# Kernel tuning notes

Measured on AMD Instinct MI355X. Metric: run time of the kernel, lower is better.

The kernel has to match this reference:

```python
import jax, jax.numpy as jnp
import numpy as np

EMBED_DIM = 768
NUM_HEADS = 12
HEAD_DIM = EMBED_DIM // NUM_HEADS
SCALE = HEAD_DIM ** -0.5
EPS = 1e-5


def _layernorm(x, g, b):
    m = jnp.mean(x, axis=-1, keepdims=True)
    v = jnp.mean(jnp.square(x - m), axis=-1, keepdims=True)
    return (x - m) * jax.lax.rsqrt(v + EPS) * g + b


def setup_inputs() -> dict:
    key = jax.random.key(0)
    ks = jax.random.split(key, 8)
    B, N, D, Hd = 16, 1024, EMBED_DIM, HEAD_DIM
    x = jax.random.normal(ks[0], (B, N, D), dtype=jnp.float32)
    W_qkv = jax.random.normal(ks[1], (D, 3 * D), dtype=jnp.float32) * (D ** -0.5)
    b_qkv = jnp.zeros((3 * D,), dtype=jnp.float32)
    W_proj = jax.random.normal(ks[2], (D, D), dtype=jnp.float32) * (D ** -0.5)
    b_proj = jnp.zeros((D,), dtype=jnp.float32)
    return {
        "x": x,
        "ln_g": jnp.ones((D,), jnp.float32), "ln_b": jnp.zeros((D,), jnp.float32),
        "W_qkv": W_qkv, "b_qkv": b_qkv,
        "qn_g": jnp.ones((Hd,), jnp.float32), "qn_b": jnp.zeros((Hd,), jnp.float32),
        "kn_g": jnp.ones((Hd,), jnp.float32), "kn_b": jnp.zeros((Hd,), jnp.float32),
        "W_proj": W_proj, "b_proj": b_proj,
    }


def reference(x, ln_g, ln_b, W_qkv, b_qkv, qn_g, qn_b, kn_g, kn_b, W_proj, b_proj):
    B, N, D = x.shape
    H, Hd = NUM_HEADS, HEAD_DIM
    xn = _layernorm(x, ln_g, ln_b)                      # qkv_norm (pre-LN of embed_dim)
    qkv = xn @ W_qkv + b_qkv                            # [B,N,3D]
    qkv = qkv.reshape(B, N, 3, H, Hd)
    q = jnp.transpose(qkv[:, :, 0], (0, 2, 1, 3))       # [B,H,N,Hd]
    k = jnp.transpose(qkv[:, :, 1], (0, 2, 1, 3))
    v = jnp.transpose(qkv[:, :, 2], (0, 2, 1, 3))
    q = _layernorm(q, qn_g, qn_b)                       # per-head QK LayerNorm
    k = _layernorm(k, kn_g, kn_b)
    attn = jnp.einsum("bhnd,bhmd->bhnm", q, k) * SCALE
    attn = jax.nn.softmax(attn, axis=-1)
    out = jnp.einsum("bhnm,bhmd->bhnd", attn, v)        # [B,H,N,Hd]
    out = jnp.transpose(out, (0, 2, 1, 3)).reshape(B, N, D)
    return out @ W_proj + b_proj
```

## Files before the change

### kernel.cpp

```cpp
#include <hip/hip_runtime.h>

typedef _Float16 half8 __attribute__((ext_vector_type(8)));
typedef _Float16 half4 __attribute__((ext_vector_type(4)));
typedef _Float16 half2v __attribute__((ext_vector_type(2)));
typedef float f32x4 __attribute__((ext_vector_type(4)));

#define B_    16
#define N_    1024
#define D_    768
#define H_    12
#define M_    (B_ * N_)
#define QKVN_ 2304
#define EPS_  1e-5f
#define QS_   0.18033688011112042f

__device__ __forceinline__ float exp2_fast(float x) {
#if __has_builtin(__builtin_amdgcn_exp2f)
    return __builtin_amdgcn_exp2f(x);
#else
    return __builtin_exp2f(x);
#endif
}

__device__ __forceinline__ size_t pk(int t16, int kc, int lg, int p, int e) {
    return ((size_t)(t16 * 24 + kc) * 4 + lg) * 128 + p * 8 + e;
}

__global__ __launch_bounds__(256) void convert_w(const float* __restrict__ Wqkv,
                                                 const float* __restrict__ Wproj,
                                                 _Float16* __restrict__ wqkv_p,
                                                 _Float16* __restrict__ wproj_p) {
    int idx = blockIdx.x * 256 + threadIdx.x;
    const int n1 = D_ * QKVN_;
    int k, n; float v; _Float16* dst;
    if (idx < n1) { k = idx / QKVN_; n = idx % QKVN_; v = Wqkv[idx]; dst = wqkv_p; }
    else { int r = idx - n1; k = r / D_; n = r % D_; v = Wproj[r]; dst = wproj_p; }
    dst[pk(n >> 4, k >> 5, (k >> 3) & 3, n & 15, k & 7)] = (_Float16)v;
}

__global__ __launch_bounds__(256) void ln_embed(const float* __restrict__ x,
                                                const float* __restrict__ g,
                                                const float* __restrict__ bb,
                                                _Float16* __restrict__ xp) {
    int row = blockIdx.x;
    int tid = threadIdx.x;
    const float2* xr = (const float2*)(x + (size_t)row * D_);
    float2 v0 = xr[tid];
    float2 v1 = make_float2(0.f, 0.f);
    if (tid < 128) v1 = xr[256 + tid];
    float s = v0.x + v0.y + v1.x + v1.y;
    float q = v0.x * v0.x + v0.y * v0.y + v1.x * v1.x + v1.y * v1.y;
#pragma unroll
    for (int m = 32; m >= 1; m >>= 1) {
        s += __shfl_xor(s, m);
        q += __shfl_xor(q, m);
    }
    __shared__ float ss[4], qq[4];
    int wave = tid >> 6;
    if ((tid & 63) == 0) { ss[wave] = s; qq[wave] = q; }
    __syncthreads();
    float S = ss[0] + ss[1] + ss[2] + ss[3];
    float Q = qq[0] + qq[1] + qq[2] + qq[3];
    float mean = S * (1.f / 768.f);
    float var  = Q * (1.f / 768.f) - mean * mean;
    float rstd = rsqrtf(var + EPS_);
    const float2* g2 = (const float2*)g;
    const float2* b2 = (const float2*)bb;
    int mt = row >> 4, p = row & 15;
    {
        int d0 = 2 * tid;
        float2 ga = g2[tid], ba = b2[tid];
        half2v w;
        w[0] = (_Float16)((v0.x - mean) * rstd * ga.x + ba.x);
        w[1] = (_Float16)((v0.y - mean) * rstd * ga.y + ba.y);
        *(half2v*)&xp[pk(mt, d0 >> 5, (d0 >> 3) & 3, p, d0 & 7)] = w;
    }
    if (tid < 128) {
        int d0 = 512 + 2 * tid;
        float2 ga = g2[256 + tid], ba = b2[256 + tid];
        half2v w;
        w[0] = (_Float16)((v1.x - mean) * rstd * ga.x + ba.x);
        w[1] = (_Float16)((v1.y - mean) * rstd * ga.y + ba.y);
        *(half2v*)&xp[pk(mt, d0 >> 5, (d0 >> 3) & 3, p, d0 & 7)] = w;
    }
}

__global__ __launch_bounds__(256, 3) void gemm_qkv(const _Float16* __restrict__ Ap,
                                                   const _Float16* __restrict__ Bp,
                                                   const float* __restrict__ bias,
                                                   const float* __restrict__ qn_g,
                                                   const float* __restrict__ qn_b,
                                                   const float* __restrict__ kn_g,
                                                   const float* __restrict__ kn_b,
                                                   _Float16* __restrict__ qo,
                                                   _Float16* __restrict__ ko,
                                                   _Float16* __restrict__ vt) {
    int xcd = blockIdx.x & 7, loc = blockIdx.x >> 3;
    int mt0 = (xcd * 16 + loc / 18) * 8;
    int nt0 = (loc % 18) * 8;
    int tid = threadIdx.x;
    int wave = tid >> 6, lane = tid & 63;
    int wm = wave >> 1, wn = wave & 1;
    int lg = lane >> 4, l15 = lane & 15;

    const _Float16* pa[4];
    const _Float16* pb[4];
#pragma unroll
    for (int i = 0; i < 4; ++i) {
        pa[i] = Ap + (size_t)(mt0 + wm * 4 + i) * 12288 + lane * 8;
        pb[i] = Bp + (size_t)(nt0 + wn * 4 + i) * 12288 + lane * 8;
    }
    f32x4 acc[4][4] = {};
    half8 a0[4], b0[4], a1[4], b1[4];
    auto ld = [&](half8 (&a)[4], half8 (&b)[4], int t) {
        int off = t * 512;
#pragma unroll
        for (int i = 0; i < 4; ++i) {
            a[i] = *(const half8*)(pa[i] + off);
            b[i] = *(const half8*)(pb[i] + off);
        }
    };
    auto mm = [&](half8 (&a)[4], half8 (&b)[4]) {
#pragma unroll
        for (int mi = 0; mi < 4; ++mi)
#pragma unroll
            for (int ni = 0; ni < 4; ++ni)
                acc[mi][ni] = __builtin_amdgcn_mfma_f32_16x16x32_f16(a[mi], b[ni], acc[mi][ni], 0, 0, 0);
    };
    ld(a0, b0, 0);
    for (int tt = 0; tt < 11; ++tt) {
        ld(a1, b1, 2 * tt + 1);
        mm(a0, b0);
        ld(a0, b0, 2 * tt + 2);
        mm(a1, b1);
    }
    ld(a1, b1, 23);
    mm(a0, b0);
    mm(a1, b1);

    int m0 = mt0 * 16, n0 = nt0 * 16;
    int col0 = n0 + wn * 64;
    int s = col0 / 768;
    int hcol = (col0 % 768) >> 6;
    float qkvb[4];
#pragma unroll
    for (int ni = 0; ni < 4; ++ni) qkvb[ni] = bias[col0 + ni * 16 + l15];

    if (s == 2) {
#pragma unroll
        for (int mi = 0; mi < 4; ++mi) {
            int r0 = m0 + wm * 64 + mi * 16 + lg * 4;
            int bidx = r0 >> 10, pos = r0 & 1023;
            int kvblk = pos >> 5, h = (pos >> 4) & 1, lgR = (pos >> 2) & 3;
            size_t vbase = ((size_t)(bidx * H_ + hcol) * 32 + kvblk) * 4;
#pragma unroll
            for (int ni = 0; ni < 4; ++ni) {
                half4 h4;
#pragma unroll
                for (int j = 0; j < 4; ++j) h4[j] = (_Float16)(acc[mi][ni][j] + qkvb[ni]);
                *(half4*)&vt[(vbase + ni) * 512 + lgR * 128 + l15 * 8 + h * 4] = h4;
            }
        }
    } else {
        const float* gg = (s == 0) ? qn_g : kn_g;
        const float* bb = (s == 0) ? qn_b : kn_b;
        float gv[4], bv[4];
#pragma unroll
        for (int ni = 0; ni < 4; ++ni) { gv[ni] = gg[ni * 16 + l15]; bv[ni] = bb[ni * 16 + l15]; }
#pragma unroll
        for (int mi = 0; mi < 4; ++mi) {
#pragma unroll
            for (int j = 0; j < 4; ++j) {
                float v[4];
                float sm = 0.f, sq = 0.f;
#pragma unroll
                for (int ni = 0; ni < 4; ++ni) {
                    v[ni] = acc[mi][ni][j] + qkvb[ni];
                    sm += v[ni];
                    sq += v[ni] * v[ni];
                }
#pragma unroll
                for (int msk = 1; msk < 16; msk <<= 1) {
                    sm += __shfl_xor(sm, msk);
                    sq += __shfl_xor(sq, msk);
                }
                float mean = sm * (1.f / 64.f);
                float var  = sq * (1.f / 64.f) - mean * mean;
                float rstd = rsqrtf(var + EPS_);
                int row = m0 + wm * 64 + mi * 16 + lg * 4 + j;
                int bidx = row >> 10, pos = row & 1023;
                if (s == 0) {
                    size_t rbase = ((size_t)(bidx * H_ + hcol) * 1024 + pos) * 64;
#pragma unroll
                    for (int ni = 0; ni < 4; ++ni) {
                        float o = (v[ni] - mean) * rstd * gv[ni] + bv[ni];
                        qo[rbase + ni * 16 + l15] = (_Float16)(o * QS_);
                    }
                } else {
                    int kvblk = pos >> 5, nh = (pos >> 4) & 1, l15R = pos & 15;
                    size_t base2 = ((size_t)(bidx * H_ + hcol) * 32 + kvblk) * 4 + nh * 2;
#pragma unroll
                    for (int ni = 0; ni < 4; ++ni) {
                        float o = (v[ni] - mean) * rstd * gv[ni] + bv[ni];
                        int ks = ni >> 1, lgR = ((ni & 1) << 1) | (l15 >> 3), elem = l15 & 7;
                        ko[(base2 + ks) * 512 + lgR * 128 + l15R * 8 + elem] = (_Float16)o;
                    }
                }
            }
        }
    }
}

struct KV {
    half8 kf[2][2];
    half8 vf[4];
};

__device__ __forceinline__ void ldKV(KV& s, const _Float16* kp, const _Float16* vp, int kvblk) {
    const _Float16* kb = kp + (size_t)kvblk * 2048;
#pragma unroll
    for (int nh = 0; nh < 2; ++nh)
#pragma unroll
        for (int ks = 0; ks < 2; ++ks)
            s.kf[nh][ks] = *(const half8*)(kb + (nh * 2 + ks) * 512);
    const _Float16* vb = vp + (size_t)kvblk * 2048;
#pragma unroll
    for (int di = 0; di < 4; ++di)
        s.vf[di] = *(const half8*)(vb + di * 512);
}

__device__ __forceinline__ void blockKV(const KV& s, const half8 (&qf)[4][2],
                                        f32x4 (&oacc)[4][4], f32x4 (&lacc)[4],
                                        half8 ones) {
#pragma unroll
    for (int mi = 0; mi < 4; ++mi) {
        f32x4 a0 = {}, a1 = {};
#pragma unroll
        for (int ks = 0; ks < 2; ++ks) {
            a0 = __builtin_amdgcn_mfma_f32_16x16x32_f16(s.kf[0][ks], qf[mi][ks], a0, 0, 0, 0);
            a1 = __builtin_amdgcn_mfma_f32_16x16x32_f16(s.kf[1][ks], qf[mi][ks], a1, 0, 0, 0);
        }
        half8 pf;
#pragma unroll
        for (int j = 0; j < 4; ++j) {
            pf[j]     = (_Float16)exp2_fast(a0[j]);
            pf[j + 4] = (_Float16)exp2_fast(a1[j]);
        }
        lacc[mi] = __builtin_amdgcn_mfma_f32_16x16x32_f16(ones, pf, lacc[mi], 0, 0, 0);
#pragma unroll
        for (int di = 0; di < 4; ++di)
            oacc[mi][di] = __builtin_amdgcn_mfma_f32_16x16x32_f16(s.vf[di], pf, oacc[mi][di], 0, 0, 0);
    }
}

__global__ __launch_bounds__(128, 2) void attn(const _Float16* __restrict__ qg,
                                               const _Float16* __restrict__ kg,
                                               const _Float16* __restrict__ vtg,
                                               _Float16* __restrict__ op) {
    int bphys = blockIdx.x;
    int jj = (bphys & 7) * 192 + (bphys >> 3);
    int bh = jj >> 3, qt = jj & 7;
    int b = bh / H_, h = bh % H_;
    int tid = threadIdx.x;
    int wid = tid >> 6, lane = tid & 63;
    int lg = lane >> 4, l15 = lane & 15;
    size_t base = (size_t)bh << 10;
    int qw0 = qt * 128 + wid * 64;

    const _Float16* qrow = qg + (base + qw0 + l15) * 64 + lg * 8;
    half8 qf[4][2];
#pragma unroll
    for (int mi = 0; mi < 4; ++mi)
#pragma unroll
        for (int ks = 0; ks < 2; ++ks)
            qf[mi][ks] = *(const half8*)(qrow + mi * 1024 + ks * 32);

    const _Float16* kp = kg + (size_t)bh * 65536 + lane * 8;
    const _Float16* vp = vtg + (size_t)bh * 65536 + lane * 8;

    half8 ones;
#pragma unroll
    for (int i = 0; i < 8; ++i) ones[i] = (_Float16)1.0f;

    f32x4 oacc[4][4] = {};
    f32x4 lacc[4] = {};

    KV s0, s1;
    ldKV(s0, kp, vp, 0);
    for (int t = 0; t < 16; ++t) {
        ldKV(s1, kp, vp, (2 * t + 1) & 31);
        blockKV(s0, qf, oacc, lacc, ones);
        ldKV(s0, kp, vp, (2 * t + 2) & 31);
        blockKV(s1, qf, oacc, lacc, ones);
    }

#pragma unroll
    for (int mi = 0; mi < 4; ++mi) {
        float inv = 1.f / lacc[mi][0];
        int mt = b * 64 + (qw0 >> 4) + mi;
#pragma unroll
        for (int di = 0; di < 4; ++di) {
            half4 h4;
#pragma unroll
            for (int j = 0; j < 4; ++j) h4[j] = (_Float16)(oacc[mi][di][j] * inv);
            *(half4*)&op[pk(mt, 2 * h + (di >> 1), (di & 1) * 2 + (lg >> 1), l15, (lg & 1) * 4)] = h4;
        }
    }
}

__global__ __launch_bounds__(256, 3) void gemm_proj(const _Float16* __restrict__ Ap,
                                                    const _Float16* __restrict__ Bp,
                                                    const float* __restrict__ bias,
                                                    float* __restrict__ out) {
    int xcd = blockIdx.x & 7, loc = blockIdx.x >> 3;
    int mt0 = (xcd * 16 + loc / 6) * 8;
    int nt0 = (loc % 6) * 8;
    int tid = threadIdx.x;
    int wave = tid >> 6, lane = tid & 63;
    int wm = wave >> 1, wn = wave & 1;
    int lg = lane >> 4, l15 = lane & 15;

    const _Float16* pa[4];
    const _Float16* pb[4];
#pragma unroll
    for (int i = 0; i < 4; ++i) {
        pa[i] = Ap + (size_t)(mt0 + wm * 4 + i) * 12288 + lane * 8;
        pb[i] = Bp + (size_t)(nt0 + wn * 4 + i) * 12288 + lane * 8;
    }
    f32x4 acc[4][4] = {};
    half8 a0[4], b0[4], a1[4], b1[4];
    auto ld = [&](half8 (&a)[4], half8 (&b)[4], int t) {
        int off = t * 512;
#pragma unroll
        for (int i = 0; i < 4; ++i) {
            a[i] = *(const half8*)(pa[i] + off);
            b[i] = *(const half8*)(pb[i] + off);
        }
    };
    auto mm = [&](half8 (&a)[4], half8 (&b)[4]) {
#pragma unroll
        for (int mi = 0; mi < 4; ++mi)
#pragma unroll
            for (int ni = 0; ni < 4; ++ni)
                acc[mi][ni] = __builtin_amdgcn_mfma_f32_16x16x32_f16(a[mi], b[ni], acc[mi][ni], 0, 0, 0);
    };
    ld(a0, b0, 0);
    for (int tt = 0; tt < 11; ++tt) {
        ld(a1, b1, 2 * tt + 1);
        mm(a0, b0);
        ld(a0, b0, 2 * tt + 2);
        mm(a1, b1);
    }
    ld(a1, b1, 23);
    mm(a0, b0);
    mm(a1, b1);

    int m0 = mt0 * 16, n0 = nt0 * 16;
#pragma unroll
    for (int mi = 0; mi < 4; ++mi)
#pragma unroll
        for (int ni = 0; ni < 4; ++ni) {
            int col = n0 + wn * 64 + ni * 16 + l15;
            float bv = bias[col];
#pragma unroll
            for (int j = 0; j < 4; ++j) {
                int row = m0 + wm * 64 + mi * 16 + lg * 4 + j;
                out[(size_t)row * D_ + col] = acc[mi][ni][j] + bv;
            }
        }
}

extern "C" void kernel_launch(void* const* d_in, const int* in_sizes, int n_in,
                              void* d_out, int out_size, void* d_ws, size_t ws_size,
                              hipStream_t stream) {
    const float* x      = (const float*)d_in[0];
    const float* ln_g   = (const float*)d_in[1];
    const float* ln_b   = (const float*)d_in[2];
    const float* W_qkv  = (const float*)d_in[3];
    const float* b_qkv  = (const float*)d_in[4];
    const float* qn_g   = (const float*)d_in[5];
    const float* qn_b   = (const float*)d_in[6];
    const float* kn_g   = (const float*)d_in[7];
    const float* kn_b   = (const float*)d_in[8];
    const float* W_proj = (const float*)d_in[9];
    const float* b_proj = (const float*)d_in[10];
    float* out = (float*)d_out;
    char* ws = (char*)d_ws;

    constexpr size_t XN_SZ    = (size_t)M_ * D_ * 2;
    constexpr size_t WQKVT_SZ = (size_t)QKVN_ * D_ * 2;
    constexpr size_t WPROJT_SZ= (size_t)D_ * D_ * 2;
    constexpr size_t HEAD_SZ  = (size_t)B_ * H_ * N_ * 64 * 2;

    _Float16* xn_p   = (_Float16*)(ws);
    _Float16* wqkv_p = (_Float16*)(ws + XN_SZ);
    _Float16* wproj_p= (_Float16*)(ws + XN_SZ + WQKVT_SZ);
    _Float16* qb     = (_Float16*)(ws + XN_SZ + WQKVT_SZ + WPROJT_SZ);
    _Float16* kb     = (_Float16*)((char*)qb + HEAD_SZ);
    _Float16* vtb    = (_Float16*)((char*)kb + HEAD_SZ);
    _Float16* ao_p   = xn_p;

    convert_w<<<9216, 256, 0, stream>>>(W_qkv, W_proj, wqkv_p, wproj_p);
    ln_embed<<<M_, 256, 0, stream>>>(x, ln_g, ln_b, xn_p);
    gemm_qkv<<<M_ / 128 * (QKVN_ / 128), 256, 0, stream>>>(xn_p, wqkv_p, b_qkv,
                                                           qn_g, qn_b, kn_g, kn_b,
                                                           qb, kb, vtb);
    attn<<<B_ * H_ * (N_ / 128), 128, 0, stream>>>(qb, kb, vtb, ao_p);
    gemm_proj<<<M_ / 128 * (D_ / 128), 256, 0, stream>>>(ao_p, wproj_p, b_proj, out);
}
```

Before: 203.1 us.

## Tile weight conversion through LDS, deepen GEMM prefetch, reorder block mapping

The weight conversion kernel now transposes 64x64 tiles through shared memory, so global reads are coalesced and each thread writes 16-byte packed vectors instead of scattered single halves. Both GEMMs move from double-buffered to triple-buffered register prefetch, holding two K-steps of loads in flight at the cost of more VGPRs. Their block-to-tile mapping is also changed so consecutive blocks on an XCD walk M first, which alters cache reuse of the A and B tiles.

```diff
diff --git a/kernel.cpp b/kernel.cpp
--- a/kernel.cpp
+++ b/kernel.cpp
@@ -30,12 +30,31 @@
                                                  const float* __restrict__ Wproj,
                                                  _Float16* __restrict__ wqkv_p,
                                                  _Float16* __restrict__ wproj_p) {
-    int idx = blockIdx.x * 256 + threadIdx.x;
-    const int n1 = D_ * QKVN_;
-    int k, n; float v; _Float16* dst;
-    if (idx < n1) { k = idx / QKVN_; n = idx % QKVN_; v = Wqkv[idx]; dst = wqkv_p; }
-    else { int r = idx - n1; k = r / D_; n = r % D_; v = Wproj[r]; dst = wproj_p; }
-    dst[pk(n >> 4, k >> 5, (k >> 3) & 3, n & 15, k & 7)] = (_Float16)v;
+    __shared__ float T[64][65];
+    int t = blockIdx.x;
+    const float* W; _Float16* O; int NW, k0, n0;
+    if (t < 432) { W = Wqkv;  O = wqkv_p;  NW = QKVN_; k0 = (t % 12) * 64; n0 = (t / 12) * 64; }
+    else { t -= 432; W = Wproj; O = wproj_p; NW = D_;  k0 = (t % 12) * 64; n0 = (t / 12) * 64; }
+    int c = threadIdx.x & 63, r4 = threadIdx.x >> 6;
+#pragma unroll
+    for (int i = 0; i < 16; ++i) {
+        int k = i * 4 + r4;
+        T[c][k] = W[(size_t)(k0 + k) * NW + n0 + c];
+    }
+    __syncthreads();
+    int g = threadIdx.x >> 5, s2 = threadIdx.x & 31;
+    int ntl = g & 3, kcl = g >> 2;
+    int nt = (n0 >> 4) + ntl, kc = (k0 >> 5) + kcl;
+#pragma unroll
+    for (int hh = 0; hh < 2; ++hh) {
+        int s = s2 + hh * 32;
+        int lg = s >> 4, p = s & 15;
+        half8 v;
+#pragma unroll
+        for (int e = 0; e < 8; ++e)
+            v[e] = (_Float16)T[ntl * 16 + p][kcl * 32 + lg * 8 + e];
+        *(half8*)&O[((size_t)(nt * 24 + kc) * 4 + lg) * 128 + p * 8] = v;
+    }
 }
 
 __global__ __launch_bounds__(256) void ln_embed(const float* __restrict__ x,
@@ -96,8 +115,8 @@
                                                    _Float16* __restrict__ ko,
                                                    _Float16* __restrict__ vt) {
     int xcd = blockIdx.x & 7, loc = blockIdx.x >> 3;
-    int mt0 = (xcd * 16 + loc / 18) * 8;
-    int nt0 = (loc % 18) * 8;
+    int mt0 = (xcd * 16 + (loc & 15)) * 8;
+    int nt0 = (loc >> 4) * 8;
     int tid = threadIdx.x;
     int wave = tid >> 6, lane = tid & 63;
     int wm = wave >> 1, wn = wave & 1;
@@ -111,7 +130,7 @@
         pb[i] = Bp + (size_t)(nt0 + wn * 4 + i) * 12288 + lane * 8;
     }
     f32x4 acc[4][4] = {};
-    half8 a0[4], b0[4], a1[4], b1[4];
+    half8 a0[4], b0[4], a1[4], b1[4], a2[4], b2[4];
     auto ld = [&](half8 (&a)[4], half8 (&b)[4], int t) {
         int off = t * 512;
 #pragma unroll
@@ -127,16 +146,15 @@
             for (int ni = 0; ni < 4; ++ni)
                 acc[mi][ni] = __builtin_amdgcn_mfma_f32_16x16x32_f16(a[mi], b[ni], acc[mi][ni], 0, 0, 0);
     };
-    ld(a0, b0, 0);
-    for (int tt = 0; tt < 11; ++tt) {
-        ld(a1, b1, 2 * tt + 1);
+    ld(a0, b0, 0); ld(a1, b1, 1);
+    for (int tt = 0; tt < 8; ++tt) {
+        ld(a2, b2, 3 * tt + 2);
         mm(a0, b0);
-        ld(a0, b0, 2 * tt + 2);
+        if (tt < 7) ld(a0, b0, 3 * tt + 3);
         mm(a1, b1);
-    }
-    ld(a1, b1, 23);
-    mm(a0, b0);
-    mm(a1, b1);
+        if (tt < 7) ld(a1, b1, 3 * tt + 4);
+        mm(a2, b2);
+    }
 
     int m0 = mt0 * 16, n0 = nt0 * 16;
     int col0 = n0 + wn * 64;
@@ -313,8 +331,8 @@
                                                     const float* __restrict__ bias,
                                                     float* __restrict__ out) {
     int xcd = blockIdx.x & 7, loc = blockIdx.x >> 3;
-    int mt0 = (xcd * 16 + loc / 6) * 8;
-    int nt0 = (loc % 6) * 8;
+    int mt0 = (xcd * 16 + (loc & 15)) * 8;
+    int nt0 = (loc >> 4) * 8;
     int tid = threadIdx.x;
     int wave = tid >> 6, lane = tid & 63;
     int wm = wave >> 1, wn = wave & 1;
@@ -328,7 +346,7 @@
         pb[i] = Bp + (size_t)(nt0 + wn * 4 + i) * 12288 + lane * 8;
     }
     f32x4 acc[4][4] = {};
-    half8 a0[4], b0[4], a1[4], b1[4];
+    half8 a0[4], b0[4], a1[4], b1[4], a2[4], b2[4];
     auto ld = [&](half8 (&a)[4], half8 (&b)[4], int t) {
         int off = t * 512;
 #pragma unroll
@@ -344,16 +362,15 @@
             for (int ni = 0; ni < 4; ++ni)
                 acc[mi][ni] = __builtin_amdgcn_mfma_f32_16x16x32_f16(a[mi], b[ni], acc[mi][ni], 0, 0, 0);
     };
-    ld(a0, b0, 0);
-    for (int tt = 0; tt < 11; ++tt) {
-        ld(a1, b1, 2 * tt + 1);
+    ld(a0, b0, 0); ld(a1, b1, 1);
+    for (int tt = 0; tt < 8; ++tt) {
+        ld(a2, b2, 3 * tt + 2);
         mm(a0, b0);
-        ld(a0, b0, 2 * tt + 2);
+        if (tt < 7) ld(a0, b0, 3 * tt + 3);
         mm(a1, b1);
-    }
-    ld(a1, b1, 23);
-    mm(a0, b0);
-    mm(a1, b1);
+        if (tt < 7) ld(a1, b1, 3 * tt + 4);
+        mm(a2, b2);
+    }
 
     int m0 = mt0 * 16, n0 = nt0 * 16;
 #pragma unroll
@@ -400,7 +417,7 @@
     _Float16* vtb    = (_Float16*)((char*)kb + HEAD_SZ);
     _Float16* ao_p   = xn_p;
 
-    convert_w<<<9216, 256, 0, stream>>>(W_qkv, W_proj, wqkv_p, wproj_p);
+    convert_w<<<576, 256, 0, stream>>>(W_qkv, W_proj, wqkv_p, wproj_p);
     ln_embed<<<M_, 256, 0, stream>>>(x, ln_g, ln_b, xn_p);
     gemm_qkv<<<M_ / 128 * (QKVN_ / 128), 256, 0, stream>>>(xn_p, wqkv_p, b_qkv,
                                                            qn_g, qn_b, kn_g, kn_b,
```

New measurement: 201.6 us. Within noise of the previous version (-0.7%).
